# Optimization experiments

Measured on AMD Instinct MI355X. Metric: run time of the kernel, lower is better.

## Reference

```python
import jax, jax.numpy as jnp
import numpy as np

B = 2048          # number of graphs
NPG = 128         # nodes per graph (hard-coded by lin1 = Linear(128*hid, 1))
N = B * NPG       # total nodes = 262144
DEG = 16          # avg degree
EPG = NPG * DEG   # edges per graph
E = B * EPG       # total edges = 4194304
IN_CH = 151
HID = 64


def setup_inputs() -> dict:
    key = jax.random.key(0)
    ks = jax.random.split(key, 6)
    x = jax.random.normal(ks[0], (N, IN_CH), jnp.float32)
    # within-graph random edges: local index in [0, NPG) plus per-graph node offset
    src_loc = jax.random.randint(ks[1], (E,), 0, NPG, dtype=jnp.int32)
    dst_loc = jax.random.randint(ks[2], (E,), 0, NPG, dtype=jnp.int32)
    off = ((jnp.arange(E, dtype=jnp.int32) // EPG) * NPG)
    edge_index = jnp.stack([src_loc + off, dst_loc + off])  # [2, E] int32
    edge_weight = jax.random.uniform(ks[3], (E,), jnp.float32)
    batch = jnp.arange(N, dtype=jnp.int32) // NPG  # sorted graph ids
    W1 = jax.random.normal(ks[4], (IN_CH, HID), jnp.float32) / np.sqrt(IN_CH)
    b1 = jnp.zeros((HID,), jnp.float32)
    Wlin = jax.random.normal(ks[5], (NPG * HID, 1), jnp.float32) / np.sqrt(NPG * HID)
    blin = jnp.zeros((1,), jnp.float32)
    return {"x": x, "edge_index": edge_index, "edge_weight": edge_weight,
            "batch": batch, "W1": W1, "b1": b1, "Wlin": Wlin, "blin": blin}


def _gcn_conv(x, row, col, w, W, b, num_nodes):
    # PyG GCNConv: h = x @ W; out[col] += dinv[row]*w*dinv[col] * h[row]; out += b
    h = x @ W                                        # [N, HID]
    deg = jax.ops.segment_sum(w, col, num_segments=num_nodes)
    dinv = jnp.where(deg > 0, jax.lax.rsqrt(deg), 0.0)
    norm = dinv[row] * w * dinv[col]                 # [E+N]
    out = jax.ops.segment_sum(h[row] * norm[:, None], col, num_segments=num_nodes)
    return out + b


def reference(x, edge_index, edge_weight, batch, W1, b1, Wlin, blin):
    num_nodes = x.shape[0]
    # add self-loops with weight 1 (GCNConv default)
    sl = jnp.arange(num_nodes, dtype=edge_index.dtype)
    row = jnp.concatenate([edge_index[0], sl])
    col = jnp.concatenate([edge_index[1], sl])
    w = jnp.concatenate([edge_weight, jnp.ones((num_nodes,), x.dtype)])
    h = jax.nn.relu(_gcn_conv(x, row, col, w, W1, b1, num_nodes))  # [N, HID]
    # linearize: nodes are batch-sorted, 128 per graph -> [B, 128*HID]
    g = h.reshape(num_nodes // NPG, NPG * h.shape[1])
    return jax.nn.sigmoid(g @ Wlin + blin)  # [B, 1]
```

## Files before the change

### kernel.cpp

```cpp
#include <hip/hip_runtime.h>
#include <math.h>

#define NPG 128
#define HID 64
#define ICH 151
#define EPG 2048
#define TPB 512
#define EPT (EPG / TPB)
#define XSS 168
#define BTS 168
#define HTS 136
#define ASS 132
#define BT_OFF 21504

typedef __attribute__((ext_vector_type(8))) short  short8;
typedef __attribute__((ext_vector_type(4))) float  floatx4;

static __device__ __forceinline__ unsigned short f2bf(float v) {
    unsigned u = __builtin_bit_cast(unsigned, v);
    return (unsigned short)((u + 0x7fffu + ((u >> 16) & 1u)) >> 16);
}

__global__ __launch_bounds__(TPB, 6) void gcn_fused(
    const float* __restrict__ x,
    const int*   __restrict__ erow,
    const int*   __restrict__ ecol,
    const float* __restrict__ ew,
    const float* __restrict__ W1,
    const float* __restrict__ b1,
    const float* __restrict__ Wlin,
    const float* __restrict__ blin,
    float* __restrict__ out)
{
    __shared__ __align__(16) char smem[43008];
    __shared__ float deg[NPG];
    __shared__ float dinv[NPG];
    __shared__ float red[TPB / 64];

    short* xs = (short*)smem;
    short* ht = (short*)smem;
    short* bt = (short*)(smem + BT_OFF);
    float* As = (float*)(smem + BT_OFF);

    const int t    = threadIdx.x;
    const int g    = blockIdx.x;
    const int lane = t & 63;
    const int wv   = t >> 6;
    const int c16  = lane & 15;
    const int kq   = (lane >> 4) * 8;

    int   er_[EPT];
    int   ec_[EPT];
    float nw_[EPT];
    const int ebase = g * EPG;
    #pragma unroll
    for (int it = 0; it < EPT; ++it) {
        int e = ebase + t + it * TPB;
        er_[it] = erow[e] & (NPG - 1);
        ec_[it] = ecol[e] & (NPG - 1);
        nw_[it] = ew[e];
    }
    if (t < NPG) deg[t] = 1.0f;

    {
        const float4* xg = (const float4*)(x + (size_t)g * (NPG * ICH));
        for (int p = t; p < NPG * ICH / 4; p += TPB) {
            float4 v = xg[p];
            int e0 = 4 * p;
            #pragma unroll
            for (int j = 0; j < 4; ++j) {
                unsigned e = (unsigned)(e0 + j);
                unsigned r = e / 151u, c = e - 151u * r;
                xs[r * XSS + c] = (short)f2bf(((const float*)&v)[j]);
            }
        }
        for (int idx = t; idx < NPG * 9; idx += TPB) {
            int r = idx / 9, c = ICH + (idx - 9 * r);
            xs[r * XSS + c] = 0;
        }
    }
    __syncthreads();

    #pragma unroll
    for (int it = 0; it < EPT; ++it)
        atomicAdd(&deg[ec_[it]], nw_[it]);

    short8 af[5];
    #pragma unroll
    for (int s = 0; s < 5; ++s)
        af[s] = *(const short8*)&xs[(wv * 16 + c16) * XSS + s * 32 + kq];
    __syncthreads();

    {
        const int c = t & 63, k0 = (t >> 6) * 2;
        for (int k = k0; k < BTS; k += 16) {
            float w0 = (k     < ICH) ? W1[k * HID + c]       : 0.0f;
            float w1 = (k + 1 < ICH) ? W1[(k + 1) * HID + c] : 0.0f;
            *(unsigned*)&bt[c * BTS + k] =
                (unsigned)f2bf(w0) | ((unsigned)f2bf(w1) << 16);
        }
    }
    if (t < NPG) dinv[t] = rsqrtf(deg[t]);
    __syncthreads();

    #pragma unroll
    for (int it = 0; it < EPT; ++it)
        nw_[it] = dinv[er_[it]] * nw_[it] * dinv[ec_[it]];

    #pragma unroll
    for (int n = 0; n < 4; ++n) {
        floatx4 acc = {0.0f, 0.0f, 0.0f, 0.0f};
        #pragma unroll
        for (int s = 0; s < 5; ++s) {
            short8 b = *(const short8*)&bt[(n * 16 + c16) * BTS + s * 32 + kq];
            acc = __builtin_amdgcn_mfma_f32_16x16x32_bf16(af[s], b, acc, 0, 0, 0);
        }
        unsigned lo = (unsigned)f2bf(acc[0]) | ((unsigned)f2bf(acc[1]) << 16);
        unsigned hi = (unsigned)f2bf(acc[2]) | ((unsigned)f2bf(acc[3]) << 16);
        int col = n * 16 + c16;
        int row = wv * 16 + (lane >> 4) * 4;
        *(int2*)&ht[col * HTS + row] = make_int2((int)lo, (int)hi);
    }
    __syncthreads();

    float partial = 0.0f;
    const int mt  = wv >> 2;
    const int nt  = wv & 3;
    const int col = nt * 16 + c16;
    const float b1v = b1[col];

    for (int q = 0; q < 4; ++q) {
        for (int p = t; p < 32 * ASS / 4; p += TPB)
            ((floatx4*)As)[p] = (floatx4){0.0f, 0.0f, 0.0f, 0.0f};
        __syncthreads();

        #pragma unroll
        for (int it = 0; it < EPT; ++it) {
            int cl = ec_[it];
            if ((cl >> 5) == q)
                atomicAdd(&As[(cl & 31) * ASS + er_[it]], nw_[it]);
        }
        if (t < 32) {
            int i = q * 32 + t;
            atomicAdd(&As[t * ASS + i], dinv[i] * dinv[i]);
        }
        __syncthreads();

        floatx4 acc = {0.0f, 0.0f, 0.0f, 0.0f};
        #pragma unroll
        for (int ks = 0; ks < 4; ++ks) {
            const float* ap = &As[(mt * 16 + c16) * ASS + ks * 32 + kq];
            floatx4 a0 = *(const floatx4*)ap;
            floatx4 a1 = *(const floatx4*)(ap + 4);
            short8 av;
            av[0] = (short)f2bf(a0[0]); av[1] = (short)f2bf(a0[1]);
            av[2] = (short)f2bf(a0[2]); av[3] = (short)f2bf(a0[3]);
            av[4] = (short)f2bf(a1[0]); av[5] = (short)f2bf(a1[1]);
            av[6] = (short)f2bf(a1[2]); av[7] = (short)f2bf(a1[3]);
            short8 b = *(const short8*)&ht[col * HTS + ks * 32 + kq];
            acc = __builtin_amdgcn_mfma_f32_16x16x32_bf16(av, b, acc, 0, 0, 0);
        }
        int node0 = q * 32 + mt * 16 + (lane >> 4) * 4;
        #pragma unroll
        for (int r = 0; r < 4; ++r) {
            float v = fmaxf(acc[r] + b1v, 0.0f);
            partial += v * Wlin[(node0 + r) * HID + col];
        }
        __syncthreads();
    }

    #pragma unroll
    for (int o = 32; o > 0; o >>= 1)
        partial += __shfl_down(partial, o, 64);
    if (lane == 0) red[wv] = partial;
    __syncthreads();
    if (t == 0) {
        float tot = blin[0];
        #pragma unroll
        for (int i = 0; i < TPB / 64; ++i) tot += red[i];
        out[g] = 1.0f / (1.0f + expf(-tot));
    }
}

extern "C" void kernel_launch(void* const* d_in, const int* in_sizes, int n_in,
                              void* d_out, int out_size, void* d_ws, size_t ws_size,
                              hipStream_t stream) {
    const float* x    = (const float*)d_in[0];
    const int*   ei   = (const int*)d_in[1];
    const float* ew   = (const float*)d_in[2];
    const float* W1   = (const float*)d_in[4];
    const float* b1   = (const float*)d_in[5];
    const float* Wlin = (const float*)d_in[6];
    const float* blin = (const float*)d_in[7];
    float* out = (float*)d_out;

    const int E = in_sizes[1] / 2;
    const int B = out_size;

    gcn_fused<<<B, TPB, 0, stream>>>(x, ei, ei + E, ew, W1, b1, Wlin, blin, out);
}
```

Measured before the change: 94.71 us.

## Load x directly into MFMA fragments, drop x staging in LDS, raise occupancy

Each lane now reads its own x row segments from global memory and packs them to bf16 register fragments, so the x tile is no longer staged through LDS. The shared buffer shrinks, launch bounds rise from 6 to 8 blocks per CU, and the degree atomics and rsqrt are moved later so they overlap the first GEMM. The aggregation loop now loads A fragments before a barrier and drops the trailing one. The per-lane x loads are strided by 151 floats and uncoalesced, which may cost global bandwidth in exchange for fewer barriers and less LDS.

```diff
diff --git a/kernel.cpp b/kernel.cpp
--- a/kernel.cpp
+++ b/kernel.cpp
@@ -7,11 +7,10 @@
 #define EPG 2048
 #define TPB 512
 #define EPT (EPG / TPB)
-#define XSS 168
 #define BTS 168
 #define HTS 136
 #define ASS 132
-#define BT_OFF 21504
+#define BT_OFF 17408
 
 typedef __attribute__((ext_vector_type(8))) short  short8;
 typedef __attribute__((ext_vector_type(4))) float  floatx4;
@@ -20,8 +19,19 @@
     unsigned u = __builtin_bit_cast(unsigned, v);
     return (unsigned short)((u + 0x7fffu + ((u >> 16) & 1u)) >> 16);
 }
-
-__global__ __launch_bounds__(TPB, 6) void gcn_fused(
+static __device__ __forceinline__ unsigned packbf(float a, float b) {
+    return (unsigned)f2bf(a) | ((unsigned)f2bf(b) << 16);
+}
+static __device__ __forceinline__ short8 pack8(const float* v) {
+    union { unsigned u[4]; short8 s; } r;
+    r.u[0] = packbf(v[0], v[1]);
+    r.u[1] = packbf(v[2], v[3]);
+    r.u[2] = packbf(v[4], v[5]);
+    r.u[3] = packbf(v[6], v[7]);
+    return r.s;
+}
+
+__global__ __launch_bounds__(TPB, 8) void gcn_fused(
     const float* __restrict__ x,
     const int*   __restrict__ erow,
     const int*   __restrict__ ecol,
@@ -32,12 +42,11 @@
     const float* __restrict__ blin,
     float* __restrict__ out)
 {
-    __shared__ __align__(16) char smem[43008];
+    __shared__ __align__(16) char smem[38912];
     __shared__ float deg[NPG];
     __shared__ float dinv[NPG];
     __shared__ float red[TPB / 64];
 
-    short* xs = (short*)smem;
     short* ht = (short*)smem;
     short* bt = (short*)(smem + BT_OFF);
     float* As = (float*)(smem + BT_OFF);
@@ -49,6 +58,8 @@
     const int c16  = lane & 15;
     const int kq   = (lane >> 4) * 8;
 
+    if (t < NPG) deg[t] = 1.0f;
+
     int   er_[EPT];
     int   ec_[EPT];
     float nw_[EPT];
@@ -60,52 +71,35 @@
         ec_[it] = ecol[e] & (NPG - 1);
         nw_[it] = ew[e];
     }
-    if (t < NPG) deg[t] = 1.0f;
-
+
+    short8 af[5];
     {
-        const float4* xg = (const float4*)(x + (size_t)g * (NPG * ICH));
-        for (int p = t; p < NPG * ICH / 4; p += TPB) {
-            float4 v = xg[p];
-            int e0 = 4 * p;
+        const float* xr = x + (size_t)g * (NPG * ICH) + (wv * 16 + c16) * ICH;
+        #pragma unroll
+        for (int s = 0; s < 5; ++s) {
+            float v[8];
             #pragma unroll
-            for (int j = 0; j < 4; ++j) {
-                unsigned e = (unsigned)(e0 + j);
-                unsigned r = e / 151u, c = e - 151u * r;
-                xs[r * XSS + c] = (short)f2bf(((const float*)&v)[j]);
+            for (int j = 0; j < 8; ++j) {
+                int k = s * 32 + kq + j;
+                v[j] = (k < ICH) ? xr[k] : 0.0f;
             }
-        }
-        for (int idx = t; idx < NPG * 9; idx += TPB) {
-            int r = idx / 9, c = ICH + (idx - 9 * r);
-            xs[r * XSS + c] = 0;
-        }
-    }
-    __syncthreads();
-
-    #pragma unroll
-    for (int it = 0; it < EPT; ++it)
-        atomicAdd(&deg[ec_[it]], nw_[it]);
-
-    short8 af[5];
-    #pragma unroll
-    for (int s = 0; s < 5; ++s)
-        af[s] = *(const short8*)&xs[(wv * 16 + c16) * XSS + s * 32 + kq];
-    __syncthreads();
+            af[s] = pack8(v);
+        }
+    }
 
     {
         const int c = t & 63, k0 = (t >> 6) * 2;
         for (int k = k0; k < BTS; k += 16) {
             float w0 = (k     < ICH) ? W1[k * HID + c]       : 0.0f;
             float w1 = (k + 1 < ICH) ? W1[(k + 1) * HID + c] : 0.0f;
-            *(unsigned*)&bt[c * BTS + k] =
-                (unsigned)f2bf(w0) | ((unsigned)f2bf(w1) << 16);
-        }
-    }
-    if (t < NPG) dinv[t] = rsqrtf(deg[t]);
+            *(unsigned*)&bt[c * BTS + k] = packbf(w0, w1);
+        }
+    }
     __syncthreads();
 
     #pragma unroll
     for (int it = 0; it < EPT; ++it)
-        nw_[it] = dinv[er_[it]] * nw_[it] * dinv[ec_[it]];
+        atomicAdd(&deg[ec_[it]], nw_[it]);
 
     #pragma unroll
     for (int n = 0; n < 4; ++n) {
@@ -115,18 +109,25 @@
             short8 b = *(const short8*)&bt[(n * 16 + c16) * BTS + s * 32 + kq];
             acc = __builtin_amdgcn_mfma_f32_16x16x32_bf16(af[s], b, acc, 0, 0, 0);
         }
-        unsigned lo = (unsigned)f2bf(acc[0]) | ((unsigned)f2bf(acc[1]) << 16);
-        unsigned hi = (unsigned)f2bf(acc[2]) | ((unsigned)f2bf(acc[3]) << 16);
         int col = n * 16 + c16;
         int row = wv * 16 + (lane >> 4) * 4;
-        *(int2*)&ht[col * HTS + row] = make_int2((int)lo, (int)hi);
-    }
-    __syncthreads();
+        *(int2*)&ht[col * HTS + row] =
+            make_int2((int)packbf(acc[0], acc[1]), (int)packbf(acc[2], acc[3]));
+    }
+    __syncthreads();
+
+    if (t < NPG) dinv[t] = rsqrtf(deg[t]);
+    __syncthreads();
+
+    #pragma unroll
+    for (int it = 0; it < EPT; ++it)
+        nw_[it] = dinv[er_[it]] * nw_[it] * dinv[ec_[it]];
 
     float partial = 0.0f;
-    const int mt  = wv >> 2;
-    const int nt  = wv & 3;
-    const int col = nt * 16 + c16;
+    const int mt   = wv >> 2;
+    const int ntb  = wv & 3;
+    const int col  = ntb * 16 + c16;
+    const int arow = mt * 16 + c16;
     const float b1v = b1[col];
 
     for (int q = 0; q < 4; ++q) {
@@ -146,19 +147,21 @@
         }
         __syncthreads();
 
-        floatx4 acc = {0.0f, 0.0f, 0.0f, 0.0f};
+        short8 afr[4];
         #pragma unroll
         for (int ks = 0; ks < 4; ++ks) {
-            const float* ap = &As[(mt * 16 + c16) * ASS + ks * 32 + kq];
+            const float* ap = &As[arow * ASS + ks * 32 + kq];
             floatx4 a0 = *(const floatx4*)ap;
             floatx4 a1 = *(const floatx4*)(ap + 4);
-            short8 av;
-            av[0] = (short)f2bf(a0[0]); av[1] = (short)f2bf(a0[1]);
-            av[2] = (short)f2bf(a0[2]); av[3] = (short)f2bf(a0[3]);
-            av[4] = (short)f2bf(a1[0]); av[5] = (short)f2bf(a1[1]);
-            av[6] = (short)f2bf(a1[2]); av[7] = (short)f2bf(a1[3]);
+            float v[8] = {a0[0], a0[1], a0[2], a0[3], a1[0], a1[1], a1[2], a1[3]};
+            afr[ks] = pack8(v);
+        }
+        __syncthreads();
+        floatx4 acc = {0.0f, 0.0f, 0.0f, 0.0f};
+        #pragma unroll
+        for (int ks = 0; ks < 4; ++ks) {
             short8 b = *(const short8*)&ht[col * HTS + ks * 32 + kq];
-            acc = __builtin_amdgcn_mfma_f32_16x16x32_bf16(av, b, acc, 0, 0, 0);
+            acc = __builtin_amdgcn_mfma_f32_16x16x32_bf16(afr[ks], b, acc, 0, 0, 0);
         }
         int node0 = q * 32 + mt * 16 + (lane >> 4) * 4;
         #pragma unroll
@@ -166,7 +169,6 @@
             float v = fmaxf(acc[r] + b1v, 0.0f);
             partial += v * Wlin[(node0 + r) * HID + col];
         }
-        __syncthreads();
     }
 
     #pragma unroll
```

After: 91.41 us. 3.5% less time.
